# Kernel optimization log

Measured on AMD Instinct MI355X. Metric: run time of the kernel, lower is better.

## Reference

```python
import jax, jax.numpy as jnp
import numpy as np

H, W = 128, 128            # image size -> n_pixels = H*W
SDP2 = 25.0                # sigma_p^2 of the RBF kernel


def setup_inputs() -> dict:
    key = jax.random.key(0)
    k1, k2, k3 = jax.random.split(key, 3)
    B, KS = 16, 21
    # pixel coordinate grid (n_pixels, 2) as (row, col)
    rr, cc = jnp.meshgrid(jnp.arange(H), jnp.arange(W), indexing='ij')
    all_pixels = jnp.stack([rr, cc], axis=-1).reshape(-1, 2).astype(jnp.float32)
    # stride-4 control grids: 32x32 = 1024 centers
    gr, gc = jnp.meshgrid(jnp.arange(0, H, 4), jnp.arange(0, W, 4), indexing='ij')
    g_centers = jnp.stack([gr, gc], axis=-1).reshape(-1, 2).astype(jnp.int32)      # (Kg, 2) int indices
    all_p_centers = g_centers.astype(jnp.float32) + 2.0                             # (M, 2) photometric centers
    Kg = g_centers.shape[0]
    M = all_p_centers.shape[0]
    betas = 0.5 * jax.random.normal(k1, (B, Kg, 2), dtype=jnp.float32)
    alphas = jax.random.normal(k2, (M, 1), dtype=jnp.float32)
    # Gaussian smoothing kernel (KS, KS)
    ax = jnp.arange(KS, dtype=jnp.float32) - (KS - 1) / 2.0
    kernel = jnp.exp(-(ax[:, None] ** 2 + ax[None, :] ** 2) / (2.0 * 9.0))
    return {"betas": betas, "alphas": alphas, "kernel": kernel,
            "all_pixels": all_pixels, "all_p_centers": all_p_centers,
            "g_centers": g_centers}


def _deformation(betas, kernel, g_centers):
    # scatter betas onto (B, 2, H, W) grid at control-point locations
    B = betas.shape[0]
    beta_img = jnp.zeros((B, 2, H, W), dtype=betas.dtype)
    rows, cols = g_centers[:, 0], g_centers[:, 1]
    beta_img = beta_img.at[:, :, rows, cols].set(jnp.transpose(betas, (0, 2, 1)))
    # depthwise 'same' conv with the shared Gaussian kernel (groups=2)
    kr, kc = kernel.shape
    big_kernel = jnp.broadcast_to(kernel, (2, 1, kr, kc))
    res = jax.lax.conv_general_dilated(
        beta_img, big_kernel, window_strides=(1, 1), padding='SAME',
        feature_group_count=2,
        dimension_numbers=('NCHW', 'OIHW', 'NCHW'))            # (B, 2, H, W)
    return jnp.transpose(res.reshape(B, 2, H * W), (0, 2, 1))  # (B, n_pixels, 2)


def reference(betas, alphas, kernel, all_pixels, all_p_centers, g_centers):
    deformation = _deformation(betas, kernel, g_centers)        # (B, N, 2)
    dp = all_pixels[None, :, :] - deformation                   # deformed pixels (B, N, 2)
    # squared-distance expansion: |dp|^2 + |c|^2 - 2 dp.c  -> (B, N, M)
    sq_dp = jnp.sum(dp * dp, axis=-1, keepdims=True)            # (B, N, 1)
    sq_c = jnp.sum(all_p_centers * all_p_centers, axis=-1)      # (M,)
    cross = jnp.einsum('bnd,md->bnm', dp, all_p_centers)        # (B, N, M)
    kmat = jnp.exp(-(sq_dp + sq_c[None, None, :] - 2.0 * cross) / (2.0 * SDP2))
    return jnp.einsum('bnm,mo->bno', kmat, alphas)              # (B, N, 1)
```

## Files before the change

### kernel.cpp

```cpp
#include <hip/hip_runtime.h>


constexpr float K_RATIO = 0.52729243f;

__global__ __launch_bounds__(256, 4) void kbpa_kernel(
    const float* __restrict__ betas,
    const float* __restrict__ alphas,
    const float* __restrict__ gker,
    float* __restrict__ out)
{
    __shared__ float  gp[32];
    __shared__ float2 sB[7][32];
    __shared__ float  sA[32 * 36];
    __shared__ float2 sT[2][40];

    const int t   = threadIdx.x;
    const int b   = blockIdx.x >> 6;
    const int r0  = (blockIdx.x & 63) << 1;
    const int trA = (r0 - 7) >> 2;

    if (t < 80) ((float2*)sT)[t] = make_float2(0.0f, 0.0f);
    if (t < 32) gp[t] = (t >= 4 && t <= 24) ? gker[210 + t - 4] : 0.0f;
    {
        const int row = t >> 3, col = (t & 7) << 2;
        *(float4*)(sA + row * 36 + col) =
            *(const float4*)(alphas + (row << 5) + col);
    }
    if (t < 224) {
        const int k = t >> 5, tc = t & 31;
        const int tr = trA + k;
        float2 v = make_float2(0.0f, 0.0f);
        if ((unsigned)tr < 32u)
            v = ((const float2*)betas)[(b << 10) + (tr << 5) + tc];
        sB[k][tc] = v;
    }
    __syncthreads();

    if (t < 64) {
        const int ty = t >> 5, tc = t & 31;
        const int r   = r0 + ty;
        const int tr0 = (r - 7) >> 2;
        const int k0  = tr0 - trA;
        float ax = 0.0f, ay = 0.0f;
#pragma unroll
        for (int k = 0; k < 6; ++k) {
            const float  w = gp[4 * (tr0 + k) - r + 14];
            const float2 v = sB[k0 + k][tc];
            ax = fmaf(w, v.x, ax);
            ay = fmaf(w, v.y, ay);
        }
        sT[ty][tc + 4] = make_float2(ax, ay);
    }
    __syncthreads();

    const int ty = t >> 7;
    const int c  = t & 127;
    const int r  = r0 + ty;

    const int tc0 = (c - 7) >> 2;
    const int dc0 = 4 * tc0 - c + 10;
    float def0 = 0.0f, def1 = 0.0f;
#pragma unroll
    for (int j = 0; j < 6; ++j) {
        const float  w = gp[dc0 + 4 * j + 4];
        const float2 v = sT[ty][tc0 + j + 4];
        def0 = fmaf(w, v.x, def0);
        def1 = fmaf(w, v.y, def1);
    }

    const float px = (float)r - def0;
    const float py = (float)c - def1;

    const int mnr = __float2int_rn((px - 2.0f) * 0.25f);
    const int m0r = min(max(mnr - 5, 0), 21);
    const int mnc = __float2int_rn((py - 2.0f) * 0.25f);
    const int m0c = min(max((mnc - 5) & ~3, 0), 16);

    float Ec[16];
    {
        const float d0 = py - (float)(4 * m0c + 2);
        float E = __expf(-d0 * d0 * 0.02f);
        float u = __expf(0.16f * d0 - 0.32f);
        Ec[0] = E;
#pragma unroll
        for (int j = 1; j < 16; ++j) { E *= u; u *= K_RATIO; Ec[j] = E; }
    }

    const float dr_ = px - (float)(4 * m0r + 2);
    float er = __expf(-dr_ * dr_ * 0.02f);
    float ur = __expf(0.16f * dr_ - 0.32f);

    float acc = 0.0f;
    const float* aBase = sA + m0r * 36 + m0c;
#pragma unroll
    for (int i = 0; i < 11; ++i) {
        float s = 0.0f;
#pragma unroll
        for (int q = 0; q < 4; ++q) {
            const float4 a = *(const float4*)(aBase + i * 36 + 4 * q);
            s = fmaf(a.x, Ec[4 * q + 0], s);
            s = fmaf(a.y, Ec[4 * q + 1], s);
            s = fmaf(a.z, Ec[4 * q + 2], s);
            s = fmaf(a.w, Ec[4 * q + 3], s);
        }
        acc = fmaf(er, s, acc);
        er *= ur; ur *= K_RATIO;
    }

    out[(b << 14) + (r << 7) + c] = acc;
}

extern "C" void kernel_launch(void* const* d_in, const int* in_sizes, int n_in,
                              void* d_out, int out_size, void* d_ws, size_t ws_size,
                              hipStream_t stream) {
    const float* betas  = (const float*)d_in[0];
    const float* alphas = (const float*)d_in[1];
    const float* gker   = (const float*)d_in[2];
    float* out = (float*)d_out;
    kbpa_kernel<<<1024, 256, 0, stream>>>(betas, alphas, gker, out);
}
```

Baseline: 65.83 us.

## Compute two rows per thread sharing alpha window loads

Each thread now computes two vertically adjacent output pixels, sharing one widened 12x20 alpha window so each LDS float4 load feeds two FMA chains. The block shrinks to 128 threads. Deformation values for both rows are packed into float4 shared entries, and the alpha tile is padded with zero columns. This trades more FMAs per pixel (240 vs 176 in the window) and higher register pressure for fewer LDS reads and half as many threads per block.

```diff
diff --git a/kernel.cpp b/kernel.cpp
--- a/kernel.cpp
+++ b/kernel.cpp
@@ -3,7 +3,7 @@
 
 constexpr float K_RATIO = 0.52729243f;
 
-__global__ __launch_bounds__(256, 4) void kbpa_kernel(
+__global__ __launch_bounds__(128, 2) void kbpa_kernel(
     const float* __restrict__ betas,
     const float* __restrict__ alphas,
     const float* __restrict__ gker,
@@ -12,22 +12,26 @@
     __shared__ float  gp[32];
     __shared__ float2 sB[7][32];
     __shared__ float  sA[32 * 36];
-    __shared__ float2 sT[2][40];
+    __shared__ float4 sT4[44];
 
     const int t   = threadIdx.x;
     const int b   = blockIdx.x >> 6;
     const int r0  = (blockIdx.x & 63) << 1;
     const int trA = (r0 - 7) >> 2;
 
-    if (t < 80) ((float2*)sT)[t] = make_float2(0.0f, 0.0f);
+    if (t < 88) ((float2*)sT4)[t] = make_float2(0.0f, 0.0f);
     if (t < 32) gp[t] = (t >= 4 && t <= 24) ? gker[210 + t - 4] : 0.0f;
     {
-        const int row = t >> 3, col = (t & 7) << 2;
+        const int row = t >> 2, col = (t & 3) << 3;
         *(float4*)(sA + row * 36 + col) =
             *(const float4*)(alphas + (row << 5) + col);
+        *(float4*)(sA + row * 36 + col + 4) =
+            *(const float4*)(alphas + (row << 5) + col + 4);
     }
-    if (t < 224) {
-        const int k = t >> 5, tc = t & 31;
+    if (t < 32)
+        *(float4*)(sA + t * 36 + 32) = make_float4(0.0f, 0.0f, 0.0f, 0.0f);
+    for (int s = t; s < 224; s += 128) {
+        const int k = s >> 5, tc = s & 31;
         const int tr = trA + k;
         float2 v = make_float2(0.0f, 0.0f);
         if ((unsigned)tr < 32u)
@@ -49,65 +53,82 @@
             ax = fmaf(w, v.x, ax);
             ay = fmaf(w, v.y, ay);
         }
-        sT[ty][tc + 4] = make_float2(ax, ay);
+        *(float2*)((float*)&sT4[tc + 4] + (ty << 1)) = make_float2(ax, ay);
     }
     __syncthreads();
 
-    const int ty = t >> 7;
-    const int c  = t & 127;
-    const int r  = r0 + ty;
+    const int c = t;
 
     const int tc0 = (c - 7) >> 2;
     const int dc0 = 4 * tc0 - c + 10;
-    float def0 = 0.0f, def1 = 0.0f;
+    float d0A = 0.0f, d1A = 0.0f, d0B = 0.0f, d1B = 0.0f;
 #pragma unroll
     for (int j = 0; j < 6; ++j) {
         const float  w = gp[dc0 + 4 * j + 4];
-        const float2 v = sT[ty][tc0 + j + 4];
-        def0 = fmaf(w, v.x, def0);
-        def1 = fmaf(w, v.y, def1);
+        const float4 v = sT4[tc0 + j + 4];
+        d0A = fmaf(w, v.x, d0A); d1A = fmaf(w, v.y, d1A);
+        d0B = fmaf(w, v.z, d0B); d1B = fmaf(w, v.w, d1B);
     }
 
-    const float px = (float)r - def0;
-    const float py = (float)c - def1;
+    const float pxA = (float)r0 - d0A,       pyA = (float)c - d1A;
+    const float pxB = (float)(r0 + 1) - d0B, pyB = (float)c - d1B;
 
-    const int mnr = __float2int_rn((px - 2.0f) * 0.25f);
-    const int m0r = min(max(mnr - 5, 0), 21);
-    const int mnc = __float2int_rn((py - 2.0f) * 0.25f);
-    const int m0c = min(max((mnc - 5) & ~3, 0), 16);
+    const int m0rA = min(max(__float2int_rn((pxA - 2.0f) * 0.25f) - 5, 0), 21);
+    const int m0rB = min(max(__float2int_rn((pxB - 2.0f) * 0.25f) - 5, 0), 21);
+    const int m0r  = min(min(m0rA, m0rB), 20);
+    const int m0cA = min(max((__float2int_rn((pyA - 2.0f) * 0.25f) - 5) & ~3, 0), 16);
+    const int m0cB = min(max((__float2int_rn((pyB - 2.0f) * 0.25f) - 5) & ~3, 0), 16);
+    const int m0c  = min(m0cA, m0cB);
 
-    float Ec[16];
+    float EcA[20], EcB[20];
     {
-        const float d0 = py - (float)(4 * m0c + 2);
+        const float d0 = pyA - (float)(4 * m0c + 2);
         float E = __expf(-d0 * d0 * 0.02f);
         float u = __expf(0.16f * d0 - 0.32f);
-        Ec[0] = E;
+        EcA[0] = E;
 #pragma unroll
-        for (int j = 1; j < 16; ++j) { E *= u; u *= K_RATIO; Ec[j] = E; }
+        for (int j = 1; j < 20; ++j) { E *= u; u *= K_RATIO; EcA[j] = E; }
+    }
+    {
+        const float d0 = pyB - (float)(4 * m0c + 2);
+        float E = __expf(-d0 * d0 * 0.02f);
+        float u = __expf(0.16f * d0 - 0.32f);
+        EcB[0] = E;
+#pragma unroll
+        for (int j = 1; j < 20; ++j) { E *= u; u *= K_RATIO; EcB[j] = E; }
     }
 
-    const float dr_ = px - (float)(4 * m0r + 2);
-    float er = __expf(-dr_ * dr_ * 0.02f);
-    float ur = __expf(0.16f * dr_ - 0.32f);
+    const float drA = pxA - (float)(4 * m0r + 2);
+    float erA = __expf(-drA * drA * 0.02f);
+    float urA = __expf(0.16f * drA - 0.32f);
+    const float drB = pxB - (float)(4 * m0r + 2);
+    float erB = __expf(-drB * drB * 0.02f);
+    float urB = __expf(0.16f * drB - 0.32f);
 
-    float acc = 0.0f;
+    float accA = 0.0f, accB = 0.0f;
     const float* aBase = sA + m0r * 36 + m0c;
 #pragma unroll
-    for (int i = 0; i < 11; ++i) {
-        float s = 0.0f;
+    for (int i = 0; i < 12; ++i) {
+        float sAcc = 0.0f, sBcc = 0.0f;
 #pragma unroll
-        for (int q = 0; q < 4; ++q) {
+        for (int q = 0; q < 5; ++q) {
             const float4 a = *(const float4*)(aBase + i * 36 + 4 * q);
-            s = fmaf(a.x, Ec[4 * q + 0], s);
-            s = fmaf(a.y, Ec[4 * q + 1], s);
-            s = fmaf(a.z, Ec[4 * q + 2], s);
-            s = fmaf(a.w, Ec[4 * q + 3], s);
+            sAcc = fmaf(a.x, EcA[4 * q + 0], sAcc);
+            sBcc = fmaf(a.x, EcB[4 * q + 0], sBcc);
+            sAcc = fmaf(a.y, EcA[4 * q + 1], sAcc);
+            sBcc = fmaf(a.y, EcB[4 * q + 1], sBcc);
+            sAcc = fmaf(a.z, EcA[4 * q + 2], sAcc);
+            sBcc = fmaf(a.z, EcB[4 * q + 2], sBcc);
+            sAcc = fmaf(a.w, EcA[4 * q + 3], sAcc);
+            sBcc = fmaf(a.w, EcB[4 * q + 3], sBcc);
         }
-        acc = fmaf(er, s, acc);
-        er *= ur; ur *= K_RATIO;
+        accA = fmaf(erA, sAcc, accA); erA *= urA; urA *= K_RATIO;
+        accB = fmaf(erB, sBcc, accB); erB *= urB; urB *= K_RATIO;
     }
 
-    out[(b << 14) + (r << 7) + c] = acc;
+    float* o = out + (b << 14) + (r0 << 7) + c;
+    o[0]   = accA;
+    o[128] = accB;
 }
 
 extern "C" void kernel_launch(void* const* d_in, const int* in_sizes, int n_in,
@@ -117,5 +138,5 @@
     const float* alphas = (const float*)d_in[1];
     const float* gker   = (const float*)d_in[2];
     float* out = (float*)d_out;
-    kbpa_kernel<<<1024, 256, 0, stream>>>(betas, alphas, gker, out);
+    kbpa_kernel<<<1024, 128, 0, stream>>>(betas, alphas, gker, out);
 }
```

Result: no change. 65.18 us (-1.0%).
